# Performance work log

Hardware: AMD Instinct MI355X
Metric: run time of the kernel (lower is better)

Reference implementation:

```python
import jax, jax.numpy as jnp
import numpy as np

NEG_INF = -9e15  # matches the torch -9000000000000000.0 mask value
LRELU_SLOPE = 0.01  # torch nn.LeakyReLU default


def setup_inputs() -> dict:
    key = jax.random.key(0)
    k1, k2, k3, k4 = jax.random.split(key, 4)
    N, F_in, F_out = 8192, 256, 128
    x = jax.random.normal(k1, (N, F_in), dtype=jnp.float32)
    adj = jax.random.randint(k2, (N, N), 0, 2, dtype=jnp.int32)
    # xavier_uniform with gain=1.414
    limW = 1.414 * np.sqrt(6.0 / (F_in + F_out))
    W = jax.random.uniform(k3, (F_in, F_out), minval=-limW, maxval=limW, dtype=jnp.float32)
    lima = 1.414 * np.sqrt(6.0 / (2 * F_out + 1))
    a = jax.random.uniform(k4, (2 * F_out, 1), minval=-lima, maxval=lima, dtype=jnp.float32)
    return {"x": x, "adj": adj, "W": W, "a": a}


def reference(x, adj, W, a):
    # h: [N, F_out]
    h = x @ W
    F_out = h.shape[1]
    a1 = a[:F_out, 0]   # attention vector for source node i
    a2 = a[F_out:, 0]   # attention vector for target node j
    # e[i, j] = leaky_relu(h_i . a1 + h_j . a2) -- equivalent to the repeat/cat
    # construction without materializing the [N, N, 2F] tensor.
    e = (h @ a1)[:, None] + (h @ a2)[None, :]  # [N, N]
    e = jnp.where(e > 0, e, LRELU_SLOPE * e)
    scores = jnp.where(adj > 0, e, NEG_INF)
    attention = jax.nn.softmax(scores, axis=1)  # dropout omitted (eval mode)
    h_prime = attention @ h  # [N, F_out]
    return jax.nn.elu(h_prime)
```

## Files before the change

### kernel.cpp

```cpp
#include <hip/hip_runtime.h>
#include <hip/hip_bf16.h>
#include <stdint.h>


#define N_NODES 8192
#define F_INF   256
#define F_OUT   128
#define LRELU   0.01f

typedef __bf16 bf16x8 __attribute__((ext_vector_type(8)));
typedef float  f32x4  __attribute__((ext_vector_type(4)));
using bf16 = __hip_bfloat16;

__device__ __forceinline__ float b2f(bf16 v) { return __bfloat162float(v); }
__device__ __forceinline__ bf16  f2b(float v) { return __float2bfloat16(v); }

__global__ __launch_bounds__(256) void k_xw(const float* __restrict__ x,
                                            const float* __restrict__ W,
                                            const float* __restrict__ a,
                                            bf16* __restrict__ hT,
                                            float* __restrict__ s1,
                                            float* __restrict__ s2) {
    __shared__ __align__(16) bf16 WT[F_OUT][F_INF + 8];
    __shared__ __align__(16) bf16 XS[64][72];
    __shared__ float waL[2 * F_INF];
    __shared__ float s1L[64], s2L[64];
    const int tid  = threadIdx.x;
    const int lane = tid & 63, wave = tid >> 6;
    const int i0   = blockIdx.x * 64;
    waL[tid] = 0.f; waL[F_INF + tid] = 0.f;
    if (tid < 64) { s1L[tid] = 0.f; s2L[tid] = 0.f; }
    __syncthreads();
    for (int idx = tid; idx < (F_INF * F_OUT) / 8; idx += 256) {
        int k  = idx >> 4;
        int n0 = (idx & 15) * 8;
        const float* src = W + (size_t)k * F_OUT + n0;
        float4 va = *(const float4*)(src);
        float4 vb = *(const float4*)(src + 4);
        float v[8] = {va.x, va.y, va.z, va.w, vb.x, vb.y, vb.z, vb.w};
        float p1 = 0.f, p2 = 0.f;
#pragma unroll
        for (int c = 0; c < 8; ++c) {
            WT[n0 + c][k] = f2b(v[c]);
            p1 += v[c] * a[n0 + c];
            p2 += v[c] * a[F_OUT + n0 + c];
        }
        atomicAdd(&waL[k], p1);
        atomicAdd(&waL[F_INF + k], p2);
    }
    __syncthreads();
    f32x4 acc[8];
#pragma unroll
    for (int t = 0; t < 8; ++t) acc[t] = {0.f, 0.f, 0.f, 0.f};
    const int m = lane & 15, quad = lane >> 4;
    const int rt = wave;
    for (int kc = 0; kc < F_INF / 64; ++kc) {
        const int k0 = kc * 64;
        {
            int part = tid & 7;
            int r    = tid >> 3;
#pragma unroll
            for (int p = 0; p < 2; ++p) {
                int rr = r + p * 32;
                const float* src = x + (size_t)(i0 + rr) * F_INF + k0 + part * 8;
                float4 va = *(const float4*)(src);
                float4 vb = *(const float4*)(src + 4);
                float v[8] = {va.x, va.y, va.z, va.w, vb.x, vb.y, vb.z, vb.w};
                __align__(16) bf16 th[8];
                float q1 = 0.f, q2 = 0.f;
#pragma unroll
                for (int c = 0; c < 8; ++c) {
                    th[c] = f2b(v[c]);
                    q1 += v[c] * waL[k0 + part * 8 + c];
                    q2 += v[c] * waL[F_INF + k0 + part * 8 + c];
                }
                *(uint4*)(&XS[rr][part * 8]) = *(const uint4*)th;
                atomicAdd(&s1L[rr], q1);
                atomicAdd(&s2L[rr], q2);
            }
        }
        __syncthreads();
#pragma unroll
        for (int ks = 0; ks < 2; ++ks) {
            bf16x8 af = *(const bf16x8*)(&XS[rt * 16 + m][ks * 32 + quad * 8]);
#pragma unroll
            for (int ct = 0; ct < 8; ++ct) {
                bf16x8 bfr = *(const bf16x8*)(&WT[ct * 16 + m][kc * 64 + ks * 32 + quad * 8]);
                acc[ct] = __builtin_amdgcn_mfma_f32_16x16x32_bf16(af, bfr, acc[ct], 0, 0, 0);
            }
        }
        __syncthreads();
    }
#pragma unroll
    for (int ct = 0; ct < 8; ++ct) {
        const int f = ct * 16 + m;
#pragma unroll
        for (int r = 0; r < 4; ++r) {
            const int i = i0 + rt * 16 + quad * 4 + r;
            hT[(size_t)f * N_NODES + i] = f2b(acc[ct][r]);
        }
    }
    if (tid < 64) { s1[i0 + tid] = s1L[tid]; s2[i0 + tid] = s2L[tid]; }
}

__global__ __launch_bounds__(256) void k_max(const float* __restrict__ s2,
                                             float* __restrict__ mg) {
    __shared__ float red[256];
    int tid = threadIdx.x;
    float m = -1e30f;
    for (int j = tid; j < N_NODES; j += 256) m = fmaxf(m, s2[j]);
    red[tid] = m;
    __syncthreads();
    for (int s = 128; s > 0; s >>= 1) {
        if (tid < s) red[tid] = fmaxf(red[tid], red[tid + s]);
        __syncthreads();
    }
    if (tid == 0) mg[0] = red[0];
}

__global__ __launch_bounds__(256) void k_attn(const int* __restrict__ adj,
                                              const float* __restrict__ s1g,
                                              const float* __restrict__ s2g,
                                              const float* __restrict__ mg,
                                              const bf16* __restrict__ hT,
                                              float* __restrict__ Of,
                                              float* __restrict__ lp) {
    __shared__ float s2s[1024];
    const int tid  = threadIdx.x;
    const int lane = tid & 63, wave = tid >> 6;
    const int m = lane & 15, quad = lane >> 4;
    const int i0    = blockIdx.x * 64;
    const int jq    = blockIdx.y;
    const int jbase = jq * 1024;
    const int irow  = i0 + wave * 16 + m;
    const float s1v = s1g[irow];
    const float tmi = s1v + mg[0];
    const float mi  = fmaxf(tmi, LRELU * tmi);
    *(float4*)&s2s[tid * 4] = *(const float4*)(s2g + jbase + tid * 4);
    const bf16* hlane = hT + (size_t)m * N_NODES + jbase + quad * 8;
    const int4* arowp = (const int4*)(adj + (size_t)irow * N_NODES + jbase);
    int4 avA[4], avB[4];
    avA[0] = arowp[quad * 2];          avA[1] = arowp[quad * 2 + 1];
    avA[2] = arowp[8 + quad * 2];      avA[3] = arowp[8 + quad * 2 + 1];
    avB[0] = arowp[16 + quad * 2];     avB[1] = arowp[16 + quad * 2 + 1];
    avB[2] = arowp[16 + 8 + quad * 2]; avB[3] = arowp[16 + 8 + quad * 2 + 1];
    uint4 hA[8], hB[8];
#pragma unroll
    for (int c = 0; c < 4; ++c)
#pragma unroll
        for (int kh = 0; kh < 2; ++kh)
            hA[c * 2 + kh] = *(const uint4*)(hlane + (size_t)(c * 16) * N_NODES + kh * 32);
    float lacc = 0.f;
    f32x4 acc[8];
#pragma unroll
    for (int c = 0; c < 8; ++c) acc[c] = {0.f, 0.f, 0.f, 0.f};
    __syncthreads();

    for (int jc = 0; jc < 16; ++jc) {
        const int jo = jc * 64;
#pragma unroll
        for (int c = 0; c < 4; ++c)
#pragma unroll
            for (int kh = 0; kh < 2; ++kh)
                hB[c * 2 + kh] = *(const uint4*)(hlane + (size_t)((c + 4) * 16) * N_NODES + jo + kh * 32);
        bf16x8 afrag[2];
#pragma unroll
        for (int kh = 0; kh < 2; ++kh) {
            const int am[8] = {avA[kh*2].x, avA[kh*2].y, avA[kh*2].z, avA[kh*2].w,
                               avA[kh*2+1].x, avA[kh*2+1].y, avA[kh*2+1].z, avA[kh*2+1].w};
            const float* s2p = &s2s[jo + kh * 32 + quad * 8];
            __align__(16) bf16 a8[8];
#pragma unroll
            for (int t = 0; t < 8; ++t) {
                float e = s1v + s2p[t];
                e = fmaxf(e, LRELU * e);
                float w = (am[t] > 0) ? __expf(e - mi) : 0.f;
                bf16 bb = f2b(w);
                a8[t] = bb;
                lacc += b2f(bb);
            }
            afrag[kh] = *(const bf16x8*)a8;
        }
#pragma unroll
        for (int q = 0; q < 4; ++q) avA[q] = avB[q];
        if (jc < 14) {
            const int base = (jc + 2) * 16;
            avB[0] = arowp[base + quad * 2];     avB[1] = arowp[base + quad * 2 + 1];
            avB[2] = arowp[base + 8 + quad * 2]; avB[3] = arowp[base + 8 + quad * 2 + 1];
        }
#pragma unroll
        for (int kh = 0; kh < 2; ++kh)
#pragma unroll
            for (int c = 0; c < 4; ++c)
                acc[c] = __builtin_amdgcn_mfma_f32_16x16x32_bf16(
                    afrag[kh], *(const bf16x8*)&hA[c * 2 + kh], acc[c], 0, 0, 0);
        if (jc < 15) {
#pragma unroll
            for (int c = 0; c < 4; ++c)
#pragma unroll
                for (int kh = 0; kh < 2; ++kh)
                    hA[c * 2 + kh] = *(const uint4*)(hlane + (size_t)(c * 16) * N_NODES + jo + 64 + kh * 32);
        }
#pragma unroll
        for (int kh = 0; kh < 2; ++kh)
#pragma unroll
            for (int c = 0; c < 4; ++c)
                acc[c + 4] = __builtin_amdgcn_mfma_f32_16x16x32_bf16(
                    afrag[kh], *(const bf16x8*)&hB[c * 2 + kh], acc[c + 4], 0, 0, 0);
    }
    lacc += __shfl_xor(lacc, 16);
    lacc += __shfl_xor(lacc, 32);
    if (quad == 0) lp[(size_t)jq * N_NODES + irow] = lacc;
#pragma unroll
    for (int c = 0; c < 8; ++c) {
        const int f = c * 16 + m;
#pragma unroll
        for (int r = 0; r < 4; ++r) {
            const int i = i0 + wave * 16 + quad * 4 + r;
            Of[((size_t)jq * N_NODES + i) * F_OUT + f] = acc[c][r];
        }
    }
}

__global__ __launch_bounds__(256) void k_comb(const float* __restrict__ Of,
                                              const float* __restrict__ lp,
                                              float* __restrict__ out) {
    size_t gid = (size_t)blockIdx.x * 256 + threadIdx.x;
    int i = (int)(gid >> 7);
    float s = 0.f, l = 0.f;
#pragma unroll
    for (int q = 0; q < 8; ++q) {
        s += Of[(size_t)q * (N_NODES * (size_t)F_OUT) + gid];
        l += lp[q * N_NODES + i];
    }
    float o = s / l;
    out[gid] = o > 0.f ? o : __expf(o) - 1.f;
}

extern "C" void kernel_launch(void* const* d_in, const int* in_sizes, int n_in,
                              void* d_out, int out_size, void* d_ws, size_t ws_size,
                              hipStream_t stream) {
    (void)out_size; (void)ws_size;
    const float* x   = nullptr;
    const int*   adj = nullptr;
    const float* W   = nullptr;
    const float* a   = nullptr;
    for (int ii = 0; ii < n_in; ++ii) {
        int sz = in_sizes[ii];
        if      (sz == N_NODES * F_INF)  x   = (const float*)d_in[ii];
        else if (sz == F_INF * F_OUT)    W   = (const float*)d_in[ii];
        else if (sz == 2 * F_OUT)        a   = (const float*)d_in[ii];
        else                             adj = (const int*)d_in[ii];
    }
    float* out = (float*)d_out;

    char* ws = (char*)d_ws;
    bf16*  hT = (bf16*)ws;  ws += (size_t)F_OUT * N_NODES * 2;
    float* s1 = (float*)ws; ws += N_NODES * 4;
    float* s2 = (float*)ws; ws += N_NODES * 4;
    float* mg = (float*)ws; ws += 256;
    float* lp = (float*)ws; ws += 8 * N_NODES * 4;
    float* Of = (float*)ws;

    k_xw  <<<N_NODES / 64, 256, 0, stream>>>(x, W, a, hT, s1, s2);
    k_max <<<1, 256, 0, stream>>>(s2, mg);
    k_attn<<<dim3(N_NODES / 64, 8), 256, 0, stream>>>(adj, s1, s2, mg, hT, Of, lp);
    k_comb<<<(N_NODES * F_OUT) / 256, 256, 0, stream>>>(Of, lp, out);
}
```

Baseline: 499.6 us.

## Shrink attention blocks to one wave and stream h fragments in small groups

The attention kernel now launches single-wave blocks of 16 rows instead of four-wave 64-row blocks. The shared-memory staging of s2 and its block barrier are gone, and s2 is read straight from global memory. The h fragments are now loaded two column-groups at a time with a one-group lookahead, replacing the 16-register A/B double buffer. This cuts register pressure to raise occupancy and removes synchronisation, but h and s2 loads are no longer shared across waves in a block and rely on cache hits.

```diff
diff --git a/kernel.cpp b/kernel.cpp
--- a/kernel.cpp
+++ b/kernel.cpp
@@ -118,61 +118,49 @@
     if (tid == 0) mg[0] = red[0];
 }
 
-__global__ __launch_bounds__(256) void k_attn(const int* __restrict__ adj,
-                                              const float* __restrict__ s1g,
-                                              const float* __restrict__ s2g,
-                                              const float* __restrict__ mg,
-                                              const bf16* __restrict__ hT,
-                                              float* __restrict__ Of,
-                                              float* __restrict__ lp) {
-    __shared__ float s2s[1024];
-    const int tid  = threadIdx.x;
-    const int lane = tid & 63, wave = tid >> 6;
+__global__ __launch_bounds__(64) void k_attn(const int* __restrict__ adj,
+                                             const float* __restrict__ s1g,
+                                             const float* __restrict__ s2g,
+                                             const float* __restrict__ mg,
+                                             const bf16* __restrict__ hT,
+                                             float* __restrict__ Of,
+                                             float* __restrict__ lp) {
+    const int lane = threadIdx.x;
     const int m = lane & 15, quad = lane >> 4;
-    const int i0    = blockIdx.x * 64;
+    const int i0    = blockIdx.x * 16;
     const int jq    = blockIdx.y;
     const int jbase = jq * 1024;
-    const int irow  = i0 + wave * 16 + m;
+    const int irow  = i0 + m;
     const float s1v = s1g[irow];
     const float tmi = s1v + mg[0];
     const float mi  = fmaxf(tmi, LRELU * tmi);
-    *(float4*)&s2s[tid * 4] = *(const float4*)(s2g + jbase + tid * 4);
-    const bf16* hlane = hT + (size_t)m * N_NODES + jbase + quad * 8;
-    const int4* arowp = (const int4*)(adj + (size_t)irow * N_NODES + jbase);
+    const bf16*  hlane = hT + (size_t)m * N_NODES + jbase + quad * 8;
+    const float* s2l   = s2g + jbase + quad * 8;
+    const int4*  arowp = (const int4*)(adj + (size_t)irow * N_NODES + jbase);
     int4 avA[4], avB[4];
     avA[0] = arowp[quad * 2];          avA[1] = arowp[quad * 2 + 1];
     avA[2] = arowp[8 + quad * 2];      avA[3] = arowp[8 + quad * 2 + 1];
     avB[0] = arowp[16 + quad * 2];     avB[1] = arowp[16 + quad * 2 + 1];
     avB[2] = arowp[16 + 8 + quad * 2]; avB[3] = arowp[16 + 8 + quad * 2 + 1];
-    uint4 hA[8], hB[8];
-#pragma unroll
-    for (int c = 0; c < 4; ++c)
-#pragma unroll
-        for (int kh = 0; kh < 2; ++kh)
-            hA[c * 2 + kh] = *(const uint4*)(hlane + (size_t)(c * 16) * N_NODES + kh * 32);
     float lacc = 0.f;
     f32x4 acc[8];
 #pragma unroll
     for (int c = 0; c < 8; ++c) acc[c] = {0.f, 0.f, 0.f, 0.f};
-    __syncthreads();
 
     for (int jc = 0; jc < 16; ++jc) {
         const int jo = jc * 64;
-#pragma unroll
-        for (int c = 0; c < 4; ++c)
-#pragma unroll
-            for (int kh = 0; kh < 2; ++kh)
-                hB[c * 2 + kh] = *(const uint4*)(hlane + (size_t)((c + 4) * 16) * N_NODES + jo + kh * 32);
         bf16x8 afrag[2];
 #pragma unroll
         for (int kh = 0; kh < 2; ++kh) {
             const int am[8] = {avA[kh*2].x, avA[kh*2].y, avA[kh*2].z, avA[kh*2].w,
                                avA[kh*2+1].x, avA[kh*2+1].y, avA[kh*2+1].z, avA[kh*2+1].w};
-            const float* s2p = &s2s[jo + kh * 32 + quad * 8];
+            float4 sa = *(const float4*)(s2l + jo + kh * 32);
+            float4 sb = *(const float4*)(s2l + jo + kh * 32 + 4);
+            const float sv[8] = {sa.x, sa.y, sa.z, sa.w, sb.x, sb.y, sb.z, sb.w};
             __align__(16) bf16 a8[8];
 #pragma unroll
             for (int t = 0; t < 8; ++t) {
-                float e = s1v + s2p[t];
+                float e = s1v + sv[t];
                 e = fmaxf(e, LRELU * e);
                 float w = (am[t] > 0) ? __expf(e - mi) : 0.f;
                 bf16 bb = f2b(w);
@@ -188,25 +176,31 @@
             avB[0] = arowp[base + quad * 2];     avB[1] = arowp[base + quad * 2 + 1];
             avB[2] = arowp[base + 8 + quad * 2]; avB[3] = arowp[base + 8 + quad * 2 + 1];
         }
+        uint4 hg[4], hn[4];
 #pragma unroll
         for (int kh = 0; kh < 2; ++kh)
 #pragma unroll
-            for (int c = 0; c < 4; ++c)
-                acc[c] = __builtin_amdgcn_mfma_f32_16x16x32_bf16(
-                    afrag[kh], *(const bf16x8*)&hA[c * 2 + kh], acc[c], 0, 0, 0);
-        if (jc < 15) {
-#pragma unroll
-            for (int c = 0; c < 4; ++c)
+            for (int c = 0; c < 2; ++c)
+                hg[c * 2 + kh] = *(const uint4*)(hlane + (size_t)(c * 16) * N_NODES + jo + kh * 32);
+#pragma unroll
+        for (int g = 0; g < 4; ++g) {
+            if (g < 3) {
+                const int cb = (g + 1) * 2;
 #pragma unroll
                 for (int kh = 0; kh < 2; ++kh)
-                    hA[c * 2 + kh] = *(const uint4*)(hlane + (size_t)(c * 16) * N_NODES + jo + 64 + kh * 32);
-        }
-#pragma unroll
-        for (int kh = 0; kh < 2; ++kh)
-#pragma unroll
-            for (int c = 0; c < 4; ++c)
-                acc[c + 4] = __builtin_amdgcn_mfma_f32_16x16x32_bf16(
-                    afrag[kh], *(const bf16x8*)&hB[c * 2 + kh], acc[c + 4], 0, 0, 0);
+#pragma unroll
+                    for (int c = 0; c < 2; ++c)
+                        hn[c * 2 + kh] = *(const uint4*)(hlane + (size_t)((cb + c) * 16) * N_NODES + jo + kh * 32);
+            }
+#pragma unroll
+            for (int kh = 0; kh < 2; ++kh)
+#pragma unroll
+                for (int c = 0; c < 2; ++c)
+                    acc[g * 2 + c] = __builtin_amdgcn_mfma_f32_16x16x32_bf16(
+                        afrag[kh], *(const bf16x8*)&hg[c * 2 + kh], acc[g * 2 + c], 0, 0, 0);
+#pragma unroll
+            for (int q = 0; q < 4; ++q) hg[q] = hn[q];
+        }
     }
     lacc += __shfl_xor(lacc, 16);
     lacc += __shfl_xor(lacc, 32);
@@ -216,7 +210,7 @@
         const int f = c * 16 + m;
 #pragma unroll
         for (int r = 0; r < 4; ++r) {
-            const int i = i0 + wave * 16 + quad * 4 + r;
+            const int i = i0 + quad * 4 + r;
             Of[((size_t)jq * N_NODES + i) * F_OUT + f] = acc[c][r];
         }
     }
@@ -264,6 +258,6 @@
 
     k_xw  <<<N_NODES / 64, 256, 0, stream>>>(x, W, a, hT, s1, s2);
     k_max <<<1, 256, 0, stream>>>(s2, mg);
-    k_attn<<<dim3(N_NODES / 64, 8), 256, 0, stream>>>(adj, s1, s2, mg, hT, Of, lp);
+    k_attn<<<dim3(N_NODES / 16, 8), 64, 0, stream>>>(adj, s1, s2, mg, hT, Of, lp);
     k_comb<<<(N_NODES * F_OUT) / 256, 256, 0, stream>>>(Of, lp, out);
 }
```

New measurement: 509.1 us. About the same (+1.9%).
